# Optimization experiments

Measured on AMD Instinct MI355X. Metric: run time of the kernel, lower is better.

## Reference

```python
import math
import jax, jax.numpy as jnp
import numpy as np

H, N2, B, L = 256, 32, 16, 8192

def setup_inputs() -> dict:
    key = jax.random.key(0)
    k_u, k_dt, k_C, k_D = jax.random.split(key, 4)
    u = jax.random.normal(k_u, (B, H, L), dtype=jnp.float32)
    log_dt = (jax.random.uniform(k_dt, (H,), dtype=jnp.float32)
              * (math.log(0.1) - math.log(0.001)) + math.log(0.001))
    log_A_real = jnp.log(0.5 * jnp.ones((H, N2), dtype=jnp.float32))
    A_imag = math.pi * jnp.broadcast_to(jnp.arange(N2, dtype=jnp.float32), (H, N2))
    C = jax.random.normal(k_C, (H, N2, 2), dtype=jnp.float32)
    D = jax.random.normal(k_D, (H,), dtype=jnp.float32)
    return {"u": u, "log_dt": log_dt, "log_A_real": log_A_real,
            "A_imag": A_imag, "C": C, "D": D}

def reference(u, log_dt, log_A_real, A_imag, C, D):
    # u: (B, H, L)
    L_ = u.shape[-1]
    dt = jnp.exp(log_dt)                              # (H,)
    Cc = C[..., 0] + 1j * C[..., 1]                   # (H, N2) complex
    A = -jnp.exp(log_A_real) + 1j * A_imag            # (H, N2) complex
    dtA = A * dt[:, None]                             # (H, N2)
    # Vandermonde: exp(dtA * l) for l in [0, L)  -> (H, N2, L)
    K_exp = jnp.exp(dtA[:, :, None] * jnp.arange(L_, dtype=jnp.float32))
    C_tilde = Cc * (jnp.exp(dtA) - 1.0) / A           # (H, N2)
    k = 2.0 * jnp.einsum('hn,hnl->hl', C_tilde, K_exp).real  # (H, L)
    # FFT convolution with zero-padding to 2L (linear conv)
    k_f = jnp.fft.rfft(k, n=2 * L_)                   # (H, L+1)
    u_f = jnp.fft.rfft(u, n=2 * L_)                   # (B, H, L+1)
    y = jnp.fft.irfft(u_f * k_f, n=2 * L_)[..., :L_]  # (B, H, L)
    y = y + u * D[:, None]
    return y
```

## Files before the change

### kernel.cpp

```cpp
#include <hip/hip_runtime.h>

#define Bk 16
#define Hk 256
#define Lk 8192
#define N2k 32
#define Tk 64
#define Gk 128
#define NSEG 8
#define SEGC 16

typedef __attribute__((ext_vector_type(8))) short short8;
typedef __attribute__((ext_vector_type(4))) float f32x4;

__device__ __forceinline__ f32x4 mfma16(short8 a, short8 b, f32x4 c) {
    return __builtin_amdgcn_mfma_f32_16x16x32_bf16(a, b, c, 0, 0, 0);
}

__device__ __forceinline__ void split1(float x, short& hi, short& lo) {
    __bf16 h = (__bf16)x;
    __bf16 l = (__bf16)(x - (float)h);
    hi = __builtin_bit_cast(short, h);
    lo = __builtin_bit_cast(short, l);
}

#define RLANE(v, i) __int_as_float(__builtin_amdgcn_readlane(__float_as_int(v), (i)))


__global__ void s4d_p0(const float* __restrict__ log_dt,
                       const float* __restrict__ log_A_real,
                       const float* __restrict__ A_imag,
                       const float* __restrict__ C,
                       double* __restrict__ MD,
                       float2* __restrict__ WS64,
                       float2* __restrict__ WS1024) {
    int t = blockIdx.x * blockDim.x + threadIdx.x;
    if (t >= Hk * N2k) return;
    int h = t >> 5;
    double dt  = exp((double)log_dt[h]);
    double are = -exp((double)log_A_real[t]);
    double aim = (double)A_imag[t];
    double dr = dt * are, di = dt * aim;
    double er = exp(dr);
    double wre = er * cos(di), wim = er * sin(di);
    double denom = are * are + aim * aim;
    double tr = wre - 1.0, ti = wim;
    double qr = (tr * are + ti * aim) / denom;
    double qi = (ti * are - tr * aim) / denom;
    double c0 = (double)C[2 * t], c1 = (double)C[2 * t + 1];
    double ctr = 2.0 * (c0 * qr - c1 * qi);
    double cti = 2.0 * (c0 * qi + c1 * qr);
    MD[4 * t] = dr; MD[4 * t + 1] = di; MD[4 * t + 2] = ctr; MD[4 * t + 3] = cti;
    double e64 = exp(64.0 * dr), a64 = 64.0 * di;
    WS64[t] = make_float2((float)(e64 * cos(a64)), (float)(e64 * sin(a64)));
    double eS = exp(1024.0 * dr), aS = 1024.0 * di;
    WS1024[t] = make_float2((float)(eS * cos(aS)), (float)(eS * sin(aS)));
}

__global__ void s4d_kvp(const double* __restrict__ MD, float* __restrict__ kpart) {
    int t = blockIdx.x * blockDim.x + threadIdx.x;
    if (t >= Hk * 64 * 4) return;
    int g = t & 3, d = (t >> 2) & 63, h = t >> 8;
    double acc = 0.0;
    #pragma unroll
    for (int j = 0; j < 8; ++j) {
        const double* md = MD + 4 * ((h << 5) + 8 * g + j);
        double e = exp((double)d * md[0]), a = (double)d * md[1];
        acc += md[2] * (e * cos(a)) - md[3] * (e * sin(a));
    }
    kpart[t] = (float)acc;
}

__global__ void s4d_kv2(const float* __restrict__ kpart, const float* __restrict__ Dv,
                        float* __restrict__ kvec) {
    int t = blockIdx.x * blockDim.x + threadIdx.x;
    if (t >= Hk * 64) return;
    int d = t & 63, h = t >> 6;
    float v = (kpart[4 * t] + kpart[4 * t + 1]) + (kpart[4 * t + 2] + kpart[4 * t + 3]);
    if (d == 0) v += Dv[h];
    kvec[t] = v;
}

__global__ void s4d_packPK(const double* __restrict__ MD,
                           const float* __restrict__ kvec,
                           short8* __restrict__ Phi, short8* __restrict__ Plo,
                           short8* __restrict__ Khi, short8* __restrict__ Klo) {
    int t = blockIdx.x * blockDim.x + threadIdx.x;
    if (t >= Hk * 512) return;
    int lane = t & 63, kh = (t >> 6) & 1, mt = (t >> 7) & 3, h = t >> 9;
    int col = mt * 16 + (lane & 15);
    int kbase = kh * 32 + ((lane >> 4) << 3);
    {
        const double* md = MD + 4 * ((h << 5) + (col >> 1));
        double dr = md[0], di = md[1];
        double er = exp(dr);
        double wre = er * cos(di), wim = er * sin(di);
        double ps = (double)(56 - kbase);
        double ezr = exp(ps * dr), ang = ps * di;
        double zr = ezr * cos(ang), zi = ezr * sin(ang);
        float pv[8];
        #pragma unroll
        for (int j = 0; j < 8; ++j) {
            pv[7 - j] = (float)((col & 1) ? zi : zr);
            double nr = zr * wre - zi * wim;
            double ni = zr * wim + zi * wre;
            zr = nr; zi = ni;
        }
        short8 hi, lo;
        #pragma unroll
        for (int e = 0; e < 8; ++e) { short a1, b1; split1(pv[e], a1, b1); hi[e] = a1; lo[e] = b1; }
        Phi[t] = hi; Plo[t] = lo;
    }
    {
        short8 hi, lo;
        #pragma unroll
        for (int e = 0; e < 8; ++e) {
            int k = kbase + e;
            float v = (k <= col) ? kvec[(h << 6) + col - k] : 0.f;
            short a1, b1; split1(v, a1, b1); hi[e] = a1; lo[e] = b1;
        }
        Khi[t] = hi; Klo[t] = lo;
    }
}

__global__ void s4d_pe2(const double* __restrict__ MD, float2* __restrict__ Ef2) {
    int t = blockIdx.x * blockDim.x + threadIdx.x;
    if (t >= Hk * 64 * 32) return;
    int n = t & 31, l = (t >> 5) & 63, h = t >> 11;
    const double* md = MD + 4 * ((h << 5) + n);
    double p = (double)(l + 1);
    double e = exp(p * md[0]), a = p * md[1];
    double re = e * cos(a), im = e * sin(a);
    double cr = md[2] * re - md[3] * im;
    double ci = md[2] * im + md[3] * re;
    Ef2[t] = make_float2((float)cr, (float)(-ci));
}

__global__ __launch_bounds__(256) void s4d_mm2(
    const float* __restrict__ u,
    const short8* __restrict__ Phi, const short8* __restrict__ Plo,
    const short8* __restrict__ Khi, const short8* __restrict__ Klo,
    const float* __restrict__ Ef,
    const float2* __restrict__ WS64, const float2* __restrict__ WS1024,
    float* __restrict__ y) {
    __shared__ __align__(16) float S[Gk * Tk];
    __shared__ float Lb[NSEG * 64];

    int b = blockIdx.x & (Bk - 1);
    int h = blockIdx.x >> 4;
    int bh = b * Hk + h;
    int tid = threadIdx.x;
    int lane = tid & 63, wv = tid >> 6;
    int lr = lane & 15, lq = lane >> 4;
    int cbase = wv * 32;
    const float* ub = u + (size_t)bh * Lk;

    short8 Uhi[2][2], Ulo[2][2];
    #pragma unroll
    for (int ct = 0; ct < 2; ++ct)
        #pragma unroll
        for (int kh = 0; kh < 2; ++kh) {
            const float* src = ub + (size_t)(cbase + ct * 16 + lr) * 64 + kh * 32 + lq * 8;
            float4 a4 = *(const float4*)src;
            float4 c4 = *(const float4*)(src + 4);
            float v[8] = {a4.x, a4.y, a4.z, a4.w, c4.x, c4.y, c4.z, c4.w};
            #pragma unroll
            for (int e = 0; e < 8; ++e) {
                short hi, lo; split1(v[e], hi, lo);
                Uhi[ct][kh][e] = hi; Ulo[ct][kh][e] = lo;
            }
        }

    #pragma unroll
    for (int mt = 0; mt < 4; ++mt) {
        int tb = (((h << 2) + mt) << 1) * 64 + lane;
        short8 Bh0 = Phi[tb], Bl0 = Plo[tb];
        short8 Bh1 = Phi[tb + 64], Bl1 = Plo[tb + 64];
        #pragma unroll
        for (int ct = 0; ct < 2; ++ct) {
            f32x4 a = {0.f, 0.f, 0.f, 0.f};
            a = mfma16(Uhi[ct][0], Bh0, a);
            a = mfma16(Ulo[ct][0], Bh0, a);
            a = mfma16(Uhi[ct][0], Bl0, a);
            a = mfma16(Uhi[ct][1], Bh1, a);
            a = mfma16(Ulo[ct][1], Bh1, a);
            a = mfma16(Uhi[ct][1], Bl1, a);
            #pragma unroll
            for (int r = 0; r < 4; ++r)
                S[(cbase + ct * 16 + lq * 4 + r) * 64 + mt * 16 + lr] = a[r];
        }
    }

    float ef[64];
    {
        const float4* er4 = (const float4*)(Ef + (((size_t)(h << 6) + lane) << 6));
        #pragma unroll
        for (int i = 0; i < 16; ++i) {
            float4 e4 = er4[i];
            ef[4 * i] = e4.x; ef[4 * i + 1] = e4.y; ef[4 * i + 2] = e4.z; ef[4 * i + 3] = e4.w;
        }
    }
    __syncthreads();

    {
        int n = tid & 31, g = tid >> 5;
        float2 W = WS64[(h << 5) + n];
        float zr = 0.f, zi = 0.f;
        for (int c = g * SEGC; c < g * SEGC + SEGC; ++c) {
            int a0 = c * 64 + 2 * n, a1 = a0 + 1;
            float vr = S[a0], vi = S[a1];
            S[a0] = zr; S[a1] = zi;
            float t_r = fmaf(W.x, zr, fmaf(-W.y, zi, vr));
            float t_i = fmaf(W.x, zi, fmaf(W.y, zr, vi));
            zr = t_r; zi = t_i;
        }
        Lb[g * 64 + 2 * n] = zr; Lb[g * 64 + 2 * n + 1] = zi;
        __syncthreads();
        if (tid < 32) {
            float2 Wseg = WS1024[(h << 5) + tid];
            float Zr = 0.f, Zi = 0.f;
            for (int g2 = 0; g2 < NSEG; ++g2) {
                float lr_ = Lb[g2 * 64 + 2 * tid], li_ = Lb[g2 * 64 + 2 * tid + 1];
                Lb[g2 * 64 + 2 * tid] = Zr; Lb[g2 * 64 + 2 * tid + 1] = Zi;
                float t_r = fmaf(Wseg.x, Zr, fmaf(-Wseg.y, Zi, lr_));
                float t_i = fmaf(Wseg.x, Zi, fmaf(Wseg.y, Zr, li_));
                Zr = t_r; Zi = t_i;
            }
        }
        __syncthreads();
        float pr = Lb[g * 64 + 2 * n], pi = Lb[g * 64 + 2 * n + 1];
        for (int c = g * SEGC; c < g * SEGC + SEGC; ++c) {
            int a0 = c * 64 + 2 * n, a1 = a0 + 1;
            S[a0] += pr; S[a1] += pi;
            float t_r = fmaf(W.x, pr, -W.y * pi);
            float t_i = fmaf(W.x, pi,  W.y * pr);
            pr = t_r; pi = t_i;
        }
    }
    __syncthreads();

    {
        float svn = S[cbase * 64 + lane];
        for (int c = cbase; c < cbase + 32; ++c) {
            float sv = svn;
            if (c + 1 < cbase + 32) svn = S[(c + 1) * 64 + lane];
            float a0 = 0.f, a1 = 0.f, a2 = 0.f, a3 = 0.f;
            #pragma unroll
            for (int m = 0; m < 64; m += 4) {
                a0 = fmaf(RLANE(sv, m + 0), ef[m + 0], a0);
                a1 = fmaf(RLANE(sv, m + 1), ef[m + 1], a1);
                a2 = fmaf(RLANE(sv, m + 2), ef[m + 2], a2);
                a3 = fmaf(RLANE(sv, m + 3), ef[m + 3], a3);
            }
            S[c * 64 + lane] = (a0 + a1) + (a2 + a3);
        }
    }
    __syncthreads();

    float* yb = y + (size_t)bh * Lk;
    #pragma unroll
    for (int ct = 0; ct < 2; ++ct) {
        #pragma unroll
        for (int mt = 0; mt < 4; ++mt) {
            int tb = (((h << 2) + mt) << 1) * 64 + lane;
            short8 Kh0 = Khi[tb],      Kl0 = Klo[tb];
            short8 Kh1 = Khi[tb + 64], Kl1 = Klo[tb + 64];
            f32x4 a = {0.f, 0.f, 0.f, 0.f};
            a = mfma16(Uhi[ct][0], Kh0, a);
            a = mfma16(Ulo[ct][0], Kh0, a);
            a = mfma16(Uhi[ct][0], Kl0, a);
            a = mfma16(Uhi[ct][1], Kh1, a);
            a = mfma16(Ulo[ct][1], Kh1, a);
            a = mfma16(Uhi[ct][1], Kl1, a);
            #pragma unroll
            for (int r = 0; r < 4; ++r) {
                int row = cbase + ct * 16 + lq * 4 + r;
                yb[(size_t)row * 64 + mt * 16 + lr] = a[r] + S[row * 64 + mt * 16 + lr];
            }
        }
    }
}

extern "C" void kernel_launch(void* const* d_in, const int* in_sizes, int n_in,
                              void* d_out, int out_size, void* d_ws, size_t ws_size,
                              hipStream_t stream) {
    const float* u          = (const float*)d_in[0];
    const float* log_dt     = (const float*)d_in[1];
    const float* log_A_real = (const float*)d_in[2];
    const float* A_imag     = (const float*)d_in[3];
    const float* C          = (const float*)d_in[4];
    const float* D          = (const float*)d_in[5];
    float* y = (float*)d_out;

    char* ws = (char*)d_ws;
    double* MD     = (double*)(ws);
    float2* WS64   = (float2*)(ws + 262144);
    float2* WS1024 = (float2*)(ws + 327680);
    float*  kpart  = (float*) (ws + 393216);
    float*  kvec   = (float*) (ws + 655360);
    short*  Phi    = (short*) (ws + 720896);
    short*  Plo    = (short*) (ws + 2818048);
    short*  Khi    = (short*) (ws + 4915200);
    short*  Klo    = (short*) (ws + 7012352);
    float*  Ef     = (float*) (ws + 9109504);

    s4d_p0<<<(Hk * N2k) / 256, 256, 0, stream>>>(log_dt, log_A_real, A_imag, C,
                                                 MD, WS64, WS1024);
    s4d_kvp<<<(Hk * 64 * 4) / 256, 256, 0, stream>>>(MD, kpart);
    s4d_kv2<<<(Hk * 64) / 256, 256, 0, stream>>>(kpart, D, kvec);
    s4d_packPK<<<(Hk * 512) / 256, 256, 0, stream>>>(MD, kvec,
                                                     (short8*)Phi, (short8*)Plo,
                                                     (short8*)Khi, (short8*)Klo);
    s4d_pe2<<<(Hk * 64 * 32) / 256, 256, 0, stream>>>(MD, (float2*)Ef);
    s4d_mm2<<<Bk * Hk, 256, 0, stream>>>(u, (const short8*)Phi, (const short8*)Plo,
                                         (const short8*)Khi, (const short8*)Klo,
                                         Ef, WS64, WS1024, y);
}
```

Baseline: 371.6 us.

## Replace readlane state-expansion FMA loop with split-bf16 MFMA fused into output GEMM

The per-chunk state-to-output expansion (S times E, 64x64 per chunk) was done with scalar FMAs and readlane broadcasts, with E held in 64 registers per thread. It is now a 3-pass hi/lo bf16 MFMA product that accumulates into the same tile as the intra-chunk K GEMM. That removes a sync, an LDS round trip and the extra add on output. A new pre-pass kernel packs E into MFMA operand layout, at the cost of one more launch and some split-bf16 precision loss.

```diff
diff --git a/kernel.cpp b/kernel.cpp
--- a/kernel.cpp
+++ b/kernel.cpp
@@ -22,8 +22,6 @@
     hi = __builtin_bit_cast(short, h);
     lo = __builtin_bit_cast(short, l);
 }
-
-#define RLANE(v, i) __int_as_float(__builtin_amdgcn_readlane(__float_as_int(v), (i)))
 
 
 __global__ void s4d_p0(const float* __restrict__ log_dt,
@@ -135,11 +133,30 @@
     Ef2[t] = make_float2((float)cr, (float)(-ci));
 }
 
-__global__ __launch_bounds__(256) void s4d_mm2(
+__global__ void s4d_packE(const float2* __restrict__ Ef2,
+                          short8* __restrict__ Ehi, short8* __restrict__ Elo) {
+    int t = blockIdx.x * blockDim.x + threadIdx.x;
+    if (t >= Hk * 512) return;
+    int lane = t & 63, kh = (t >> 6) & 1, mt = (t >> 7) & 3, h = t >> 9;
+    int col = mt * 16 + (lane & 15);
+    int kbase = kh * 32 + ((lane >> 4) << 3);
+    const float2* row = Ef2 + ((size_t)(h << 6) + col) * 32 + (kbase >> 1);
+    short8 hi, lo;
+    #pragma unroll
+    for (int q = 0; q < 4; ++q) {
+        float2 f = row[q];
+        short a1, b1;
+        split1(f.x, a1, b1); hi[2 * q] = a1;     lo[2 * q] = b1;
+        split1(f.y, a1, b1); hi[2 * q + 1] = a1; lo[2 * q + 1] = b1;
+    }
+    Ehi[t] = hi; Elo[t] = lo;
+}
+
+__global__ __launch_bounds__(256) void s4d_mm4(
     const float* __restrict__ u,
     const short8* __restrict__ Phi, const short8* __restrict__ Plo,
     const short8* __restrict__ Khi, const short8* __restrict__ Klo,
-    const float* __restrict__ Ef,
+    const short8* __restrict__ Ehi, const short8* __restrict__ Elo,
     const float2* __restrict__ WS64, const float2* __restrict__ WS1024,
     float* __restrict__ y) {
     __shared__ __align__(16) float S[Gk * Tk];
@@ -187,16 +204,6 @@
             #pragma unroll
             for (int r = 0; r < 4; ++r)
                 S[(cbase + ct * 16 + lq * 4 + r) * 64 + mt * 16 + lr] = a[r];
-        }
-    }
-
-    float ef[64];
-    {
-        const float4* er4 = (const float4*)(Ef + (((size_t)(h << 6) + lane) << 6));
-        #pragma unroll
-        for (int i = 0; i < 16; ++i) {
-            float4 e4 = er4[i];
-            ef[4 * i] = e4.x; ef[4 * i + 1] = e4.y; ef[4 * i + 2] = e4.z; ef[4 * i + 3] = e4.w;
         }
     }
     __syncthreads();
@@ -238,32 +245,29 @@
     }
     __syncthreads();
 
-    {
-        float svn = S[cbase * 64 + lane];
-        for (int c = cbase; c < cbase + 32; ++c) {
-            float sv = svn;
-            if (c + 1 < cbase + 32) svn = S[(c + 1) * 64 + lane];
-            float a0 = 0.f, a1 = 0.f, a2 = 0.f, a3 = 0.f;
+    float* yb = y + (size_t)bh * Lk;
+    #pragma unroll
+    for (int ct = 0; ct < 2; ++ct) {
+        short8 Shi[2], Slo[2];
+        #pragma unroll
+        for (int kh = 0; kh < 2; ++kh) {
+            const float* src = &S[(cbase + ct * 16 + lr) * 64 + kh * 32 + lq * 8];
+            float4 g0 = *(const float4*)src;
+            float4 g1 = *(const float4*)(src + 4);
+            float v[8] = {g0.x, g0.y, g0.z, g0.w, g1.x, g1.y, g1.z, g1.w};
             #pragma unroll
-            for (int m = 0; m < 64; m += 4) {
-                a0 = fmaf(RLANE(sv, m + 0), ef[m + 0], a0);
-                a1 = fmaf(RLANE(sv, m + 1), ef[m + 1], a1);
-                a2 = fmaf(RLANE(sv, m + 2), ef[m + 2], a2);
-                a3 = fmaf(RLANE(sv, m + 3), ef[m + 3], a3);
+            for (int e = 0; e < 8; ++e) {
+                short hi, lo; split1(v[e], hi, lo);
+                Shi[kh][e] = hi; Slo[kh][e] = lo;
             }
-            S[c * 64 + lane] = (a0 + a1) + (a2 + a3);
-        }
-    }
-    __syncthreads();
-
-    float* yb = y + (size_t)bh * Lk;
-    #pragma unroll
-    for (int ct = 0; ct < 2; ++ct) {
+        }
         #pragma unroll
         for (int mt = 0; mt < 4; ++mt) {
             int tb = (((h << 2) + mt) << 1) * 64 + lane;
             short8 Kh0 = Khi[tb],      Kl0 = Klo[tb];
             short8 Kh1 = Khi[tb + 64], Kl1 = Klo[tb + 64];
+            short8 Eh0 = Ehi[tb],      El0 = Elo[tb];
+            short8 Eh1 = Ehi[tb + 64], El1 = Elo[tb + 64];
             f32x4 a = {0.f, 0.f, 0.f, 0.f};
             a = mfma16(Uhi[ct][0], Kh0, a);
             a = mfma16(Ulo[ct][0], Kh0, a);
@@ -271,10 +275,16 @@
             a = mfma16(Uhi[ct][1], Kh1, a);
             a = mfma16(Ulo[ct][1], Kh1, a);
             a = mfma16(Uhi[ct][1], Kl1, a);
+            a = mfma16(Shi[0], Eh0, a);
+            a = mfma16(Slo[0], Eh0, a);
+            a = mfma16(Shi[0], El0, a);
+            a = mfma16(Shi[1], Eh1, a);
+            a = mfma16(Slo[1], Eh1, a);
+            a = mfma16(Shi[1], El1, a);
             #pragma unroll
             for (int r = 0; r < 4; ++r) {
                 int row = cbase + ct * 16 + lq * 4 + r;
-                yb[(size_t)row * 64 + mt * 16 + lr] = a[r] + S[row * 64 + mt * 16 + lr];
+                yb[(size_t)row * 64 + mt * 16 + lr] = a[r];
             }
         }
     }
@@ -301,7 +311,9 @@
     short*  Plo    = (short*) (ws + 2818048);
     short*  Khi    = (short*) (ws + 4915200);
     short*  Klo    = (short*) (ws + 7012352);
-    float*  Ef     = (float*) (ws + 9109504);
+    float2* Ef2    = (float2*)(ws + 9109504);
+    short*  Ehi    = (short*) (ws + 13303808);
+    short*  Elo    = (short*) (ws + 15400960);
 
     s4d_p0<<<(Hk * N2k) / 256, 256, 0, stream>>>(log_dt, log_A_real, A_imag, C,
                                                  MD, WS64, WS1024);
@@ -310,8 +322,10 @@
     s4d_packPK<<<(Hk * 512) / 256, 256, 0, stream>>>(MD, kvec,
                                                      (short8*)Phi, (short8*)Plo,
                                                      (short8*)Khi, (short8*)Klo);
-    s4d_pe2<<<(Hk * 64 * 32) / 256, 256, 0, stream>>>(MD, (float2*)Ef);
-    s4d_mm2<<<Bk * Hk, 256, 0, stream>>>(u, (const short8*)Phi, (const short8*)Plo,
+    s4d_pe2<<<(Hk * 64 * 32) / 256, 256, 0, stream>>>(MD, Ef2);
+    s4d_packE<<<(Hk * 512) / 256, 256, 0, stream>>>(Ef2, (short8*)Ehi, (short8*)Elo);
+    s4d_mm4<<<Bk * Hk, 256, 0, stream>>>(u, (const short8*)Phi, (const short8*)Plo,
                                          (const short8*)Khi, (const short8*)Klo,
-                                         Ef, WS64, WS1024, y);
-}
+                                         (const short8*)Ehi, (const short8*)Elo,
+                                         WS64, WS1024, y);
+}
```

After: 321.1 us. 13.6% less time.
